# Optimization experiments

Measured on AMD Instinct MI355X. Metric: run time of the kernel, lower is better.

The kernel has to match this reference:

```python
import jax, jax.numpy as jnp
import numpy as np

B, S, D, H = 2, 2048, 1024, 16
DH = D // H  # dim_per_head = 64


def setup_inputs() -> dict:
    key = jax.random.key(0)
    ks = jax.random.split(key, 12)
    std = 1.0 / np.sqrt(D)
    inp = {
        "key": jax.random.normal(ks[0], (B, S, D), jnp.float32),
        "value": jax.random.normal(ks[1], (B, S, D), jnp.float32),
        "query": jax.random.normal(ks[2], (B, S, D), jnp.float32),
        "mask": jax.random.randint(ks[3], (B, S, S), 0, 2) == 1,
        "Wk": jax.random.normal(ks[4], (D, D), jnp.float32) * std,
        "bk": jnp.zeros((D,), jnp.float32),
        "Wv": jax.random.normal(ks[5], (D, D), jnp.float32) * std,
        "bv": jnp.zeros((D,), jnp.float32),
        "Wq": jax.random.normal(ks[6], (D, D), jnp.float32) * std,
        "bq": jnp.zeros((D,), jnp.float32),
        "Wo": jax.random.normal(ks[7], (D, D), jnp.float32) * std,
        "bo": jnp.zeros((D,), jnp.float32),
    }
    return inp


def _shape(x):
    # (B, L, D) -> (B, H, L, DH)
    return x.reshape(B, -1, H, DH).transpose(0, 2, 1, 3)


def reference(key, value, query, mask, Wk, bk, Wv, bv, Wq, bq, Wo, bo):
    k = _shape(key @ Wk.T + bk)      # (B,H,S,DH)
    v = _shape(value @ Wv.T + bv)    # (B,H,S,DH)
    q = _shape(query @ Wq.T + bq)    # (B,H,S,DH)
    q = q / jnp.sqrt(jnp.asarray(DH, q.dtype))
    scores = jnp.einsum("bhqd,bhkd->bhqk", q, k).astype(jnp.float32)
    scores = jnp.where(mask[:, None, :, :], jnp.float32(-1e18), scores)
    attn = jax.nn.softmax(scores, axis=-1).astype(q.dtype)  # (B,H,S,S)
    # dropout p=0.0 -> identity
    ctx = jnp.einsum("bhqk,bhkd->bhqd", attn, v)
    ctx = ctx.transpose(0, 2, 1, 3).reshape(B, -1, D)
    output = ctx @ Wo.T + bo
    top_attn = attn[:, 0, :, :]
    return output, top_attn
```

## Files before the change

### kernel.cpp

```cpp
#include <hip/hip_runtime.h>

constexpr int BB = 2, SS = 2048, DD = 1024, HH = 16, DHH = 64;

typedef __attribute__((ext_vector_type(4))) float f32x4;
typedef __attribute__((ext_vector_type(8))) __bf16 bf16x8;
typedef __attribute__((ext_vector_type(8))) unsigned short us8;

__device__ __forceinline__ unsigned short f32_to_bf16(float f) {
    unsigned int u = __float_as_uint(f);
    u += 0x7fffu + ((u >> 16) & 1u);
    return (unsigned short)(u >> 16);
}

__device__ __forceinline__ ushort2 pk_bf16(float a, float b) {
#if __has_builtin(__builtin_amdgcn_cvt_pk_bf16_f32)
    typedef __attribute__((ext_vector_type(2))) __bf16 bf16x2;
    bf16x2 r = __builtin_amdgcn_cvt_pk_bf16_f32(a, b);
    return *(ushort2*)&r;
#else
    ushort2 r; r.x = f32_to_bf16(a); r.y = f32_to_bf16(b); return r;
#endif
}
__device__ __forceinline__ ushort4 pk_bf16x4(float a, float b, float c, float d) {
    const ushort2 lo = pk_bf16(a, b), hi = pk_bf16(c, d);
    ushort4 r; r.x = lo.x; r.y = lo.y; r.z = hi.x; r.w = hi.y;
    return r;
}
__device__ __forceinline__ us8 cvt_us8(float4 a, float4 b) {
    const ushort4 lo = pk_bf16x4(a.x, a.y, a.z, a.w);
    const ushort4 hi = pk_bf16x4(b.x, b.y, b.z, b.w);
    us8 o;
    o[0] = lo.x; o[1] = lo.y; o[2] = lo.z; o[3] = lo.w;
    o[4] = hi.x; o[5] = hi.y; o[6] = hi.z; o[7] = hi.w;
    return o;
}

__device__ __forceinline__ f32x4 mfma_bf16(bf16x8 a, bf16x8 b, f32x4 c) {
    return __builtin_amdgcn_mfma_f32_16x16x32_bf16(a, b, c, 0, 0, 0);
}

__device__ __forceinline__ void stage16(const void* g, void* l) {
    typedef const __attribute__((address_space(1))) unsigned int gas_t;
    typedef __attribute__((address_space(3))) unsigned int las_t;
    __builtin_amdgcn_global_load_lds((gas_t*)(unsigned long long)g,
                                     (las_t*)(unsigned int)(unsigned long long)l,
                                     16, 0, 0);
}

__device__ __forceinline__ void cvt_block(const float* __restrict__ src,
                                          unsigned short* __restrict__ dst, int blk) {
    const size_t i = ((size_t)blk * 256 + threadIdx.x) * 8;
    const float4 a = *(const float4*)(src + i);
    const float4 b = *(const float4*)(src + i + 4);
    *(us8*)(dst + i) = cvt_us8(a, b);
}

__global__ __launch_bounds__(256) void cvt_bf16(const float* __restrict__ src,
                                                unsigned short* __restrict__ dst) {
    cvt_block(src, dst, blockIdx.x);
}

__global__ __launch_bounds__(256) void prep(const float* __restrict__ q,
                                            const float* __restrict__ k,
                                            const float* __restrict__ Wq,
                                            const float* __restrict__ Wk,
                                            const float* __restrict__ Wv,
                                            unsigned short* __restrict__ Xq,
                                            unsigned short* __restrict__ Xk,
                                            unsigned short* __restrict__ Wqb,
                                            unsigned short* __restrict__ Wkb,
                                            unsigned short* __restrict__ Wvb,
                                            const int* __restrict__ mask,
                                            unsigned long long* __restrict__ pm) {
    const int id = blockIdx.x;
    if (id < 4096) {
        const int sel = id >> 11, blk = id & 2047;
        cvt_block(sel == 0 ? q : k, sel == 0 ? Xq : Xk, blk);
    } else if (id < 5632) {
        const int wid = id - 4096;
        const int sel = wid >> 9, blk = wid & 511;
        cvt_block(sel == 0 ? Wq : (sel == 1 ? Wk : Wv),
                  sel == 0 ? Wqb : (sel == 1 ? Wkb : Wvb), blk);
    } else {
        const int mid = id - 5632;
        const int t = threadIdx.x, lane = t & 63;
#pragma unroll
        for (int it = 0; it < 4; ++it) {
            const size_t chunk = (size_t)mid * 16 + it * 4 + (t >> 6);
            const int val = mask[chunk * 64 + lane];
            const unsigned long long b = __ballot(val != 0);
            if (lane == 0) pm[chunk] = b;
        }
    }
}

__global__ __launch_bounds__(512) void gemm_qkv(
    const unsigned short* __restrict__ Xq, const unsigned short* __restrict__ Xk,
    const float* __restrict__ Vf,
    const unsigned short* __restrict__ Wqb, const unsigned short* __restrict__ Wkb,
    const unsigned short* __restrict__ Wvb,
    const float* __restrict__ bq, const float* __restrict__ bk,
    const float* __restrict__ bv,
    unsigned short* __restrict__ qws, unsigned short* __restrict__ kws,
    unsigned short* __restrict__ vws,
    unsigned short* __restrict__ q0, unsigned short* __restrict__ k0,
    float qscale) {
    constexpr int K = DD;
    __shared__ __align__(16) unsigned short AB[2][2][128][64];

    const int id = blockIdx.x;
    const int nid = (id & 7) * 96 + (id >> 3);
    const int which = nid >> 8;
    const int r8 = nid & 255;
    const int m0 = (r8 >> 3) * 128;
    const int n0 = (r8 & 7) * 128;

    const int t = threadIdx.x;
    const int lane = t & 63, w = t >> 6;
    const int l15 = lane & 15, quad = lane >> 4;
    const int wm = (w >> 2) * 64, wn = (w & 3) * 32;
    const bool vp = (which == 2);

    const unsigned short* Ab = which == 0 ? Xq : Xk;
    const unsigned short* Wb = which == 0 ? Wqb : (which == 1 ? Wkb : Wvb);
    const float* bias = which == 0 ? bq : (which == 1 ? bk : bv);
    const float scale = which == 0 ? qscale : 1.0f;

    const int srow = lane >> 3;
    const int scol8 = ((lane & 7) ^ srow) * 8;
    const unsigned short* Agp = Ab + (size_t)(m0 + w * 8 + srow) * K + scol8;
    const unsigned short* Bgp = Wb + (size_t)(n0 + w * 8 + srow) * K + scol8;

    const int vrow = t >> 3, vc = t & 7;
    const float* Vg = Vf + (size_t)(m0 + vrow) * K + vc * 8;

    f32x4 acc[4][2] = {};
    float4 va0, va1, va2, va3;

    if (!vp) {
#pragma unroll
        for (int j = 0; j < 2; ++j) {
            stage16(Agp + (size_t)(j * 64) * K, &AB[0][0][w * 8 + j * 64][0]);
            stage16(Bgp + (size_t)(j * 64) * K, &AB[1][0][w * 8 + j * 64][0]);
        }
    } else {
        va0 = *(const float4*)(Vg);
        va1 = *(const float4*)(Vg + 4);
        va2 = *(const float4*)(Vg + (size_t)64 * K);
        va3 = *(const float4*)(Vg + (size_t)64 * K + 4);
#pragma unroll
        for (int j = 0; j < 2; ++j)
            stage16(Bgp + (size_t)(j * 64) * K, &AB[1][0][w * 8 + j * 64][0]);
        {
            const int wr0 = vrow, wr1 = 64 + vrow;
            *(us8*)((unsigned char*)&AB[0][0][0][0] + wr0 * 128 + ((vc ^ (wr0 & 7)) * 16))
                = cvt_us8(va0, va1);
            *(us8*)((unsigned char*)&AB[0][0][0][0] + wr1 * 128 + ((vc ^ (wr1 & 7)) * 16))
                = cvt_us8(va2, va3);
        }
        __asm__ volatile("s_waitcnt lgkmcnt(0)" ::: "memory");
    }

    for (int kk = 0; kk < K / 64; ++kk) {
        const int cur = kk & 1;
        if (kk < K / 64 - 1) {
            const size_t ko = (size_t)(kk + 1) * 64;
            if (!vp) {
#pragma unroll
                for (int j = 0; j < 2; ++j) {
                    stage16(Agp + (size_t)(j * 64) * K + ko, &AB[0][cur ^ 1][w * 8 + j * 64][0]);
                    stage16(Bgp + (size_t)(j * 64) * K + ko, &AB[1][cur ^ 1][w * 8 + j * 64][0]);
                }
                __asm__ volatile("s_waitcnt vmcnt(4)" ::: "memory");
            } else {
                va0 = *(const float4*)(Vg + ko);
                va1 = *(const float4*)(Vg + ko + 4);
                va2 = *(const float4*)(Vg + (size_t)64 * K + ko);
                va3 = *(const float4*)(Vg + (size_t)64 * K + ko + 4);
#pragma unroll
                for (int j = 0; j < 2; ++j)
                    stage16(Bgp + (size_t)(j * 64) * K + ko, &AB[1][cur ^ 1][w * 8 + j * 64][0]);
                __asm__ volatile("s_waitcnt vmcnt(6)" ::: "memory");
            }
        } else {
            __asm__ volatile("s_waitcnt vmcnt(0)" ::: "memory");
        }
        __builtin_amdgcn_s_barrier();
        __builtin_amdgcn_sched_barrier(0);

#pragma unroll
        for (int s = 0; s < 2; ++s) {
            const int ch = ((s * 4 + quad) ^ (l15 & 7)) * 8;
            bf16x8 af[4], bfr[2];
#pragma unroll
            for (int mi = 0; mi < 4; ++mi)
                af[mi] = *(const bf16x8*)&AB[0][cur][wm + mi * 16 + l15][ch];
#pragma unroll
            for (int ni = 0; ni < 2; ++ni)
                bfr[ni] = *(const bf16x8*)&AB[1][cur][wn + ni * 16 + l15][ch];
            __builtin_amdgcn_s_setprio(1);
#pragma unroll
            for (int mi = 0; mi < 4; ++mi)
#pragma unroll
                for (int ni = 0; ni < 2; ++ni)
                    acc[mi][ni] = mfma_bf16(af[mi], bfr[ni], acc[mi][ni]);
            __builtin_amdgcn_s_setprio(0);
        }

        if (vp && kk < K / 64 - 1) {
            const int wr0 = vrow, wr1 = 64 + vrow;
            *(us8*)((unsigned char*)&AB[0][cur ^ 1][0][0] + wr0 * 128 + ((vc ^ (wr0 & 7)) * 16))
                = cvt_us8(va0, va1);
            *(us8*)((unsigned char*)&AB[0][cur ^ 1][0][0] + wr1 * 128 + ((vc ^ (wr1 & 7)) * 16))
                = cvt_us8(va2, va3);
            __asm__ volatile("s_waitcnt lgkmcnt(0)" ::: "memory");
        }

        __builtin_amdgcn_sched_barrier(0);
        __builtin_amdgcn_s_barrier();
        __builtin_amdgcn_sched_barrier(0);
    }

    if (which < 2) {
        unsigned short* o = which == 0 ? qws : kws;
        unsigned short* h0 = which == 0 ? q0 : k0;
#pragma unroll
        for (int ni = 0; ni < 2; ++ni) {
            const int c = n0 + wn + ni * 16 + l15;
            const float bs = bias[c];
            const int hi2 = c >> 6, di = c & (DHH - 1);
#pragma unroll
            for (int mi = 0; mi < 4; ++mi) {
#pragma unroll
                for (int r = 0; r < 4; ++r) {
                    const int mrow = m0 + wm + mi * 16 + quad * 4 + r;
                    const int bi2 = mrow >> 11, si = mrow & (SS - 1);
                    const unsigned short v16 = f32_to_bf16((acc[mi][ni][r] + bs) * scale);
                    o[((size_t)(bi2 * HH + hi2) * SS + si) * DHH + di] = v16;
                    if (hi2 == 0)
                        h0[((size_t)bi2 * SS + si) * DHH + di] = v16;
                }
            }
        }
    } else {
        unsigned short* scr = (unsigned short*)&AB[0][0][0][0] + w * (32 * 72);
#pragma unroll
        for (int ni = 0; ni < 2; ++ni) {
            const int c = n0 + wn + ni * 16 + l15;
            const float bs = bias[c];
#pragma unroll
            for (int mi = 0; mi < 4; ++mi)
                *(ushort4*)&scr[(ni * 16 + l15) * 72 + mi * 16 + quad * 4] =
                    pk_bf16x4(acc[mi][ni][0] + bs, acc[mi][ni][1] + bs,
                              acc[mi][ni][2] + bs, acc[mi][ni][3] + bs);
        }
        __asm__ volatile("s_waitcnt lgkmcnt(0)" ::: "memory");
        const int mb = m0 + wm;
        const int bi2 = mb >> 11, si0 = mb & (SS - 1);
        const int rowc = lane & 7;
#pragma unroll
        for (int k2 = 0; k2 < 4; ++k2) {
            const int col = k2 * 8 + (lane >> 3);
            const us8 vv = *(const us8*)&scr[col * 72 + rowc * 8];
            const int c = n0 + wn + col;
            *(us8*)&vws[((size_t)(bi2 * HH + (c >> 6)) * DHH + (c & 63)) * SS
                        + si0 + rowc * 8] = vv;
        }
    }
}

__global__ __launch_bounds__(512) void gemm_o(const unsigned short* __restrict__ A,
                                              const unsigned short* __restrict__ Wb,
                                              const float* __restrict__ bias,
                                              float* __restrict__ outp) {
    constexpr int K = DD;
    __shared__ __align__(16) unsigned short AB[2][2][128][64];

    const int id = blockIdx.x;
    const int nid = (id & 7) * 32 + (id >> 3);
    const int m0 = (nid >> 3) * 128;
    const int n0 = (nid & 7) * 128;

    const int t = threadIdx.x;
    const int lane = t & 63, w = t >> 6;
    const int l15 = lane & 15, quad = lane >> 4;
    const int wm = (w >> 2) * 64, wn = (w & 3) * 32;

    const int srow = lane >> 3;
    const int scol8 = ((lane & 7) ^ srow) * 8;
    const unsigned short* Agp = A + (size_t)(m0 + w * 8 + srow) * K + scol8;
    const unsigned short* Bgp = Wb + (size_t)(n0 + w * 8 + srow) * K + scol8;

    f32x4 acc[4][2] = {};

#pragma unroll
    for (int j = 0; j < 2; ++j) {
        stage16(Agp + (size_t)(j * 64) * K, &AB[0][0][w * 8 + j * 64][0]);
        stage16(Bgp + (size_t)(j * 64) * K, &AB[1][0][w * 8 + j * 64][0]);
    }

    for (int kk = 0; kk < K / 64; ++kk) {
        const int cur = kk & 1;
        if (kk < K / 64 - 1) {
            const size_t ko = (size_t)(kk + 1) * 64;
#pragma unroll
            for (int j = 0; j < 2; ++j) {
                stage16(Agp + (size_t)(j * 64) * K + ko, &AB[0][cur ^ 1][w * 8 + j * 64][0]);
                stage16(Bgp + (size_t)(j * 64) * K + ko, &AB[1][cur ^ 1][w * 8 + j * 64][0]);
            }
            __asm__ volatile("s_waitcnt vmcnt(4)" ::: "memory");
        } else {
            __asm__ volatile("s_waitcnt vmcnt(0)" ::: "memory");
        }
        __builtin_amdgcn_s_barrier();
        __builtin_amdgcn_sched_barrier(0);

#pragma unroll
        for (int s = 0; s < 2; ++s) {
            const int ch = ((s * 4 + quad) ^ (l15 & 7)) * 8;
            bf16x8 af[4], bfr[2];
#pragma unroll
            for (int mi = 0; mi < 4; ++mi)
                af[mi] = *(const bf16x8*)&AB[0][cur][wm + mi * 16 + l15][ch];
#pragma unroll
            for (int ni = 0; ni < 2; ++ni)
                bfr[ni] = *(const bf16x8*)&AB[1][cur][wn + ni * 16 + l15][ch];
            __builtin_amdgcn_s_setprio(1);
#pragma unroll
            for (int mi = 0; mi < 4; ++mi)
#pragma unroll
                for (int ni = 0; ni < 2; ++ni)
                    acc[mi][ni] = mfma_bf16(af[mi], bfr[ni], acc[mi][ni]);
            __builtin_amdgcn_s_setprio(0);
        }
        __builtin_amdgcn_sched_barrier(0);
        __builtin_amdgcn_s_barrier();
        __builtin_amdgcn_sched_barrier(0);
    }

#pragma unroll
    for (int ni = 0; ni < 2; ++ni) {
        const int c = n0 + wn + ni * 16 + l15;
        const float bs = bias[c];
#pragma unroll
        for (int mi = 0; mi < 4; ++mi)
#pragma unroll
            for (int r = 0; r < 4; ++r) {
                const int mrow = m0 + wm + mi * 16 + quad * 4 + r;
                outp[(size_t)mrow * DD + c] = acc[mi][ni][r] + bs;
            }
    }
}

__global__ __launch_bounds__(512, 4) void flash_attn(const unsigned short* __restrict__ qws,
                                                     const unsigned short* __restrict__ kws,
                                                     const unsigned short* __restrict__ vws,
                                                     const unsigned long long* __restrict__ pm,
                                                     unsigned short* __restrict__ ctx,
                                                     float2* __restrict__ stats) {
    __shared__ __align__(16) unsigned short Ksh[2][64][64];
    __shared__ __align__(16) unsigned short Vsh[2][64][64];
    __shared__ __align__(16) unsigned short Psh[8][16][72];

    constexpr int NQT = SS / 128;
    const int id = blockIdx.x;
    const int nid = (id & 7) * 64 + (id >> 3);
    const int qt = nid % NQT;
    const int bh = nid / NQT;
    const int bi = bh / HH, hi = bh % HH;

    const int t = threadIdx.x;
    const int lane = t & 63, w = t >> 6;
    const int l15 = lane & 15, quad = lane >> 4;
    const int sh4 = quad * 4;
    const int xk = quad ^ (l15 & 7);

    const unsigned short* qp = qws + (size_t)bh * SS * DHH;
    const unsigned short* kp = kws + (size_t)bh * SS * DHH;
    const unsigned short* vp = vws + (size_t)bh * DHH * SS;

    const int q_loc = qt * 128 + w * 16 + l15;
    const bf16x8 bq0 = *(const bf16x8*)(qp + (size_t)q_loc * DHH + quad * 8);
    const bf16x8 bq1 = *(const bf16x8*)(qp + (size_t)q_loc * DHH + 32 + quad * 8);
    const unsigned long long* pmrow = pm + ((size_t)bi * SS + q_loc) * (SS / 64);

    const int srow = lane >> 3;
    const int scol = (lane & 7) ^ srow;
    const unsigned short* kg = kp + (size_t)(w * 8 + srow) * DHH + scol * 8;
    const unsigned short* vg = vp + (size_t)(w * 8 + srow) * SS + scol * 8;

    f32x4 accO[4] = {};
    float m_run = -1e30f, l_run = 0.f;
    const float NEG_INF = -__builtin_inff();

    unsigned long long mcur = pmrow[0];
    stage16(kg, &Ksh[0][w * 8][0]);
    stage16(vg, &Vsh[0][w * 8][0]);

    constexpr int NT = SS / 64;
    for (int kt = 0; kt < NT; ++kt) {
        const int cur = kt & 1;
        unsigned long long mnxt = 0;
        if (kt < NT - 1) {
            mnxt = pmrow[kt + 1];
            stage16(kg + (size_t)(kt + 1) * 64 * DHH, &Ksh[cur ^ 1][w * 8][0]);
            stage16(vg + (size_t)(kt + 1) * 64,       &Vsh[cur ^ 1][w * 8][0]);
            __asm__ volatile("s_waitcnt vmcnt(3)" ::: "memory");
        } else {
            __asm__ volatile("s_waitcnt vmcnt(0)" ::: "memory");
        }
        __builtin_amdgcn_s_barrier();
        __builtin_amdgcn_sched_barrier(0);

        const unsigned short* Kb = &Ksh[cur][0][0];
        const unsigned short* Vb = &Vsh[cur][0][0];

        bf16x8 ak0[4], ak1[4];
#pragma unroll
        for (int i = 0; i < 4; ++i) {
            ak0[i] = *(const bf16x8*)&Kb[(i * 16 + l15) * 64 + xk * 8];
            ak1[i] = *(const bf16x8*)&Kb[(i * 16 + l15) * 64 + (xk ^ 4) * 8];
        }

        const unsigned int mlo = ((unsigned int)mcur) >> sh4;
        const unsigned int mhi = ((unsigned int)(mcur >> 32)) >> sh4;

        float sc[4][4];
        __builtin_amdgcn_s_setprio(1);
#pragma unroll
        for (int i = 0; i < 4; ++i) {
            f32x4 s4 = {};
            s4 = mfma_bf16(ak0[i], bq0, s4);
            s4 = mfma_bf16(ak1[i], bq1, s4);
            const unsigned int mw = (i & 2) ? mhi : mlo;
#pragma unroll
            for (int r = 0; r < 4; ++r)
                sc[i][r] = ((mw >> ((i & 1) * 16 + r)) & 1u) ? NEG_INF : s4[r];
        }
        __builtin_amdgcn_s_setprio(0);

        bf16x8 av0[4], av1[4];
#pragma unroll
        for (int i = 0; i < 4; ++i) {
            av0[i] = *(const bf16x8*)&Vb[(i * 16 + l15) * 64 + xk * 8];
            av1[i] = *(const bf16x8*)&Vb[(i * 16 + l15) * 64 + (xk ^ 4) * 8];
        }

        float tm = sc[0][0];
#pragma unroll
        for (int i = 0; i < 4; ++i)
#pragma unroll
            for (int r = 0; r < 4; ++r) tm = fmaxf(tm, sc[i][r]);
        tm = fmaxf(tm, __shfl_xor(tm, 16));
        tm = fmaxf(tm, __shfl_xor(tm, 32));

        const bool nodefer = !__all(tm <= m_run + 8.0f);
        const float mn = nodefer ? fmaxf(m_run, tm) : m_run;

        float rs = 0.f;
#pragma unroll
        for (int i = 0; i < 4; ++i)
#pragma unroll
            for (int r = 0; r < 4; ++r) {
                const float p = __builtin_amdgcn_exp2f(sc[i][r] - mn);
                sc[i][r] = p;
                rs += p;
            }
        rs += __shfl_xor(rs, 16);
        rs += __shfl_xor(rs, 32);

        if (nodefer) {
            const float alpha = __builtin_amdgcn_exp2f(m_run - mn);
            l_run = l_run * alpha + rs;
            m_run = mn;
#pragma unroll
            for (int i = 0; i < 4; ++i) accO[i] *= alpha;
        } else {
            l_run += rs;
        }

#pragma unroll
        for (int i = 0; i < 4; ++i)
            *(ushort4*)&Psh[w][l15][i * 16 + sh4] =
                pk_bf16x4(sc[i][0], sc[i][1], sc[i][2], sc[i][3]);
        __asm__ volatile("s_waitcnt lgkmcnt(0)" ::: "memory");

        const bf16x8 p0 = *(const bf16x8*)&Psh[w][l15][quad * 8];
        const bf16x8 p1 = *(const bf16x8*)&Psh[w][l15][32 + quad * 8];
        __builtin_amdgcn_s_setprio(1);
#pragma unroll
        for (int i = 0; i < 4; ++i) {
            accO[i] = mfma_bf16(av0[i], p0, accO[i]);
            accO[i] = mfma_bf16(av1[i], p1, accO[i]);
        }
        __builtin_amdgcn_s_setprio(0);

        __builtin_amdgcn_sched_barrier(0);
        __builtin_amdgcn_s_barrier();
        __builtin_amdgcn_sched_barrier(0);
        mcur = mnxt;
    }

    const float inv = 1.0f / l_run;
    unsigned short* cb = ctx + ((size_t)(bi * SS) + q_loc) * DD + hi * DHH;
#pragma unroll
    for (int i = 0; i < 4; ++i)
        *(ushort4*)&cb[i * 16 + sh4] = pk_bf16x4(accO[i][0] * inv, accO[i][1] * inv,
                                                 accO[i][2] * inv, accO[i][3] * inv);

    if (hi == 0 && quad == 0) {
        float2 st; st.x = m_run; st.y = l_run;
        stats[(size_t)bi * SS + q_loc] = st;
    }
}

__global__ __launch_bounds__(256) void prob_h0(const unsigned short* __restrict__ q0,
                                               const unsigned short* __restrict__ k0,
                                               const unsigned long long* __restrict__ pm,
                                               const float2* __restrict__ stats,
                                               float* __restrict__ outp) {
    __shared__ __align__(16) unsigned short Ksh[64][72];

    const int id = blockIdx.x;
    const int nid = (id & 7) * 64 + (id >> 3);
    const int kc = nid & 7;
    const int qt = (nid >> 3) & 31;
    const int bi = nid >> 8;

    const int t = threadIdx.x;
    const int lane = t & 63, w = t >> 6;
    const int l15 = lane & 15, quad = lane >> 4;
    const int sh4 = quad * 4;

    const int q = qt * 64 + w * 16 + l15;
    const unsigned short* qp = q0 + ((size_t)bi * SS + q) * DHH;
    const bf16x8 bq0 = *(const bf16x8*)(qp + quad * 8);
    const bf16x8 bq1 = *(const bf16x8*)(qp + 32 + quad * 8);

    const unsigned short* kp = k0 + (size_t)bi * SS * DHH;
    const unsigned long long* pmq = pm + ((size_t)bi * SS + q) * (SS / 64);
    float* orow = outp + ((size_t)bi * SS + q) * SS;

    const float2 st = stats[(size_t)bi * SS + q];
    const float M = st.x;
    const float invL = 1.0f / st.y;

    for (int kt = 0; kt < 4; ++kt) {
        const int key0 = kc * 256 + kt * 64;
        __syncthreads();
#pragma unroll
        for (int hf = 0; hf < 2; ++hf) {
            const int v = t + hf * 256;
            const int row = v >> 3, off = (v & 7) * 8;
            *(us8*)&Ksh[row][off] = *(const us8*)(kp + (size_t)(key0 + row) * DHH + off);
        }
        __syncthreads();

        const unsigned long long m64 = pmq[kc * 4 + kt];
        const unsigned int mlo = ((unsigned int)m64) >> sh4;
        const unsigned int mhi = ((unsigned int)(m64 >> 32)) >> sh4;

#pragma unroll
        for (int i = 0; i < 4; ++i) {
            const bf16x8 ak0 = *(const bf16x8*)&Ksh[i * 16 + l15][quad * 8];
            const bf16x8 ak1 = *(const bf16x8*)&Ksh[i * 16 + l15][32 + quad * 8];
            f32x4 s4 = {};
            s4 = mfma_bf16(ak0, bq0, s4);
            s4 = mfma_bf16(ak1, bq1, s4);
            const unsigned int mw = (i & 2) ? mhi : mlo;
            float4 ov;
#pragma unroll
            for (int r = 0; r < 4; ++r) {
                const float p = __builtin_amdgcn_exp2f(s4[r] - M) * invL;
                ((float*)&ov)[r] = ((mw >> ((i & 1) * 16 + r)) & 1u) ? 0.0f : p;
            }
            *(float4*)&orow[key0 + i * 16 + sh4] = ov;
        }
    }
}

extern "C" void kernel_launch(void* const* d_in, const int* in_sizes, int n_in,
                              void* d_out, int out_size, void* d_ws, size_t ws_size,
                              hipStream_t stream) {
    const float* key_   = (const float*)d_in[0];
    const float* value_ = (const float*)d_in[1];
    const float* query_ = (const float*)d_in[2];
    const int*   mask_  = (const int*)d_in[3];
    const float* Wk = (const float*)d_in[4];
    const float* bk = (const float*)d_in[5];
    const float* Wv = (const float*)d_in[6];
    const float* bv = (const float*)d_in[7];
    const float* Wq = (const float*)d_in[8];
    const float* bq = (const float*)d_in[9];
    const float* Wo = (const float*)d_in[10];
    const float* bo = (const float*)d_in[11];

    constexpr size_t XS  = (size_t)BB * SS * DD;
    constexpr size_t WSZ = (size_t)DD * DD;

    float* out_f = (float*)d_out;
    unsigned short* scratch = (unsigned short*)(out_f + XS);
    unsigned short* qws = scratch;
    unsigned short* kws = qws + XS;
    unsigned short* vws = kws + XS;
    unsigned short* ctx = vws + XS;

    unsigned short* q0 = (unsigned short*)d_ws;
    unsigned short* k0 = q0 + (size_t)BB * SS * DHH;
    unsigned long long* pm = (unsigned long long*)(k0 + (size_t)BB * SS * DHH);
    float2* stats = (float2*)(pm + (size_t)BB * SS * (SS / 64));

    unsigned short* Xq  = (unsigned short*)out_f;
    unsigned short* Xk  = Xq + XS;
    unsigned short* Wqb = ctx;
    unsigned short* Wkb = Wqb + WSZ;
    unsigned short* Wvb = Wkb + WSZ;
    unsigned short* Wob = qws;

    const float qscale = 0.125f * 1.4426950408889634f;

    prep<<<13824, 256, 0, stream>>>(query_, key_, Wq, Wk, Wv,
                                    Xq, Xk, Wqb, Wkb, Wvb, mask_, pm);

    gemm_qkv<<<768, 512, 0, stream>>>(Xq, Xk, value_, Wqb, Wkb, Wvb,
                                      bq, bk, bv, qws, kws, vws, q0, k0, qscale);

    flash_attn<<<BB * HH * (SS / 128), 512, 0, stream>>>(qws, kws, vws, pm, ctx, stats);

    cvt_bf16<<<WSZ / 2048, 256, 0, stream>>>(Wo, Wob);

    gemm_o<<<256, 512, 0, stream>>>(ctx, Wob, bo, out_f);

    prob_h0<<<512, 256, 0, stream>>>(q0, k0, pm, stats, out_f + XS);
}
```

Before: 308.9 us.

## Restructure QKV GEMM to 4-wave single-buffered tiles and split O-proj into 128x64 tiles

gemm_qkv now runs 256 threads per block with four waves, each computing a 64x64 output sub-tile (4x4 MFMA accumulators) from a single-buffered LDS tile. The intent is more blocks resident per CU (launch bounds 256,3) in place of software double buffering. gemm_o moves to 128x64 output tiles with 256 threads and 512 blocks, which fills more CUs. The cost is that global loads are no longer overlapped with MFMA inside a block; the design relies on occupancy across blocks to hide that latency.

```diff
diff --git a/kernel.cpp b/kernel.cpp
--- a/kernel.cpp
+++ b/kernel.cpp
@@ -94,7 +94,7 @@
     }
 }
 
-__global__ __launch_bounds__(512) void gemm_qkv(
+__global__ __launch_bounds__(256, 3) void gemm_qkv(
     const unsigned short* __restrict__ Xq, const unsigned short* __restrict__ Xk,
     const float* __restrict__ Vf,
     const unsigned short* __restrict__ Wqb, const unsigned short* __restrict__ Wkb,
@@ -106,7 +106,9 @@
     unsigned short* __restrict__ q0, unsigned short* __restrict__ k0,
     float qscale) {
     constexpr int K = DD;
-    __shared__ __align__(16) unsigned short AB[2][2][128][64];
+    __shared__ __align__(16) unsigned char LDSU[36864];
+    unsigned short* Ash = (unsigned short*)LDSU;
+    unsigned short* Bsh = Ash + 128 * 64;
 
     const int id = blockIdx.x;
     const int nid = (id & 7) * 96 + (id >> 3);
@@ -116,74 +118,51 @@
     const int n0 = (r8 & 7) * 128;
 
     const int t = threadIdx.x;
-    const int lane = t & 63, w = t >> 6;
+    const int lane = t & 63;
     const int l15 = lane & 15, quad = lane >> 4;
-    const int wm = (w >> 2) * 64, wn = (w & 3) * 32;
+    const int w = t >> 6, wr = w >> 1, wc = w & 1;
     const bool vp = (which == 2);
 
-    const unsigned short* Ab = which == 0 ? Xq : Xk;
+    const unsigned short* Ap = which == 0 ? Xq : Xk;
     const unsigned short* Wb = which == 0 ? Wqb : (which == 1 ? Wkb : Wvb);
     const float* bias = which == 0 ? bq : (which == 1 ? bk : bv);
     const float scale = which == 0 ? qscale : 1.0f;
 
-    const int srow = lane >> 3;
-    const int scol8 = ((lane & 7) ^ srow) * 8;
-    const unsigned short* Agp = Ab + (size_t)(m0 + w * 8 + srow) * K + scol8;
-    const unsigned short* Bgp = Wb + (size_t)(n0 + w * 8 + srow) * K + scol8;
-
-    const int vrow = t >> 3, vc = t & 7;
-    const float* Vg = Vf + (size_t)(m0 + vrow) * K + vc * 8;
-
-    f32x4 acc[4][2] = {};
-    float4 va0, va1, va2, va3;
-
-    if (!vp) {
-#pragma unroll
-        for (int j = 0; j < 2; ++j) {
-            stage16(Agp + (size_t)(j * 64) * K, &AB[0][0][w * 8 + j * 64][0]);
-            stage16(Bgp + (size_t)(j * 64) * K, &AB[1][0][w * 8 + j * 64][0]);
-        }
-    } else {
-        va0 = *(const float4*)(Vg);
-        va1 = *(const float4*)(Vg + 4);
-        va2 = *(const float4*)(Vg + (size_t)64 * K);
-        va3 = *(const float4*)(Vg + (size_t)64 * K + 4);
-#pragma unroll
-        for (int j = 0; j < 2; ++j)
-            stage16(Bgp + (size_t)(j * 64) * K, &AB[1][0][w * 8 + j * 64][0]);
-        {
-            const int wr0 = vrow, wr1 = 64 + vrow;
-            *(us8*)((unsigned char*)&AB[0][0][0][0] + wr0 * 128 + ((vc ^ (wr0 & 7)) * 16))
-                = cvt_us8(va0, va1);
-            *(us8*)((unsigned char*)&AB[0][0][0][0] + wr1 * 128 + ((vc ^ (wr1 & 7)) * 16))
-                = cvt_us8(va2, va3);
-        }
-        __asm__ volatile("s_waitcnt lgkmcnt(0)" ::: "memory");
-    }
+    const int srow = t >> 3;
+    const int scol8 = ((t & 7) ^ (srow & 7)) * 8;
+    const unsigned short* Agp = Ap + (size_t)(m0 + srow) * K + scol8;
+    const unsigned short* Bgp = Wb + (size_t)(n0 + srow) * K + scol8;
+    const float* Vgp = Vf + (size_t)(m0 + srow) * K + scol8;
+    char* ldst = (char*)LDSU + t * 16;
+
+    f32x4 acc[4][4] = {};
 
     for (int kk = 0; kk < K / 64; ++kk) {
-        const int cur = kk & 1;
-        if (kk < K / 64 - 1) {
-            const size_t ko = (size_t)(kk + 1) * 64;
-            if (!vp) {
-#pragma unroll
-                for (int j = 0; j < 2; ++j) {
-                    stage16(Agp + (size_t)(j * 64) * K + ko, &AB[0][cur ^ 1][w * 8 + j * 64][0]);
-                    stage16(Bgp + (size_t)(j * 64) * K + ko, &AB[1][cur ^ 1][w * 8 + j * 64][0]);
-                }
-                __asm__ volatile("s_waitcnt vmcnt(4)" ::: "memory");
-            } else {
-                va0 = *(const float4*)(Vg + ko);
-                va1 = *(const float4*)(Vg + ko + 4);
-                va2 = *(const float4*)(Vg + (size_t)64 * K + ko);
-                va3 = *(const float4*)(Vg + (size_t)64 * K + ko + 4);
-#pragma unroll
-                for (int j = 0; j < 2; ++j)
-                    stage16(Bgp + (size_t)(j * 64) * K + ko, &AB[1][cur ^ 1][w * 8 + j * 64][0]);
-                __asm__ volatile("s_waitcnt vmcnt(6)" ::: "memory");
+        const size_t ko = (size_t)kk * 64;
+        if (!vp) {
+#pragma unroll
+            for (int j = 0; j < 4; ++j)
+                stage16(Agp + (size_t)(j * 32) * K + ko, ldst + j * 4096);
+#pragma unroll
+            for (int j = 0; j < 4; ++j)
+                stage16(Bgp + (size_t)(j * 32) * K + ko, ldst + 16384 + j * 4096);
+            __asm__ volatile("s_waitcnt vmcnt(0)" ::: "memory");
+        } else {
+            float4 va[8];
+#pragma unroll
+            for (int j = 0; j < 4; ++j) {
+                const float* vsrc = Vgp + (size_t)(j * 32) * K + ko;
+                va[2 * j]     = *(const float4*)vsrc;
+                va[2 * j + 1] = *(const float4*)(vsrc + 4);
             }
-        } else {
+#pragma unroll
+            for (int j = 0; j < 4; ++j)
+                stage16(Bgp + (size_t)(j * 32) * K + ko, ldst + 16384 + j * 4096);
             __asm__ volatile("s_waitcnt vmcnt(0)" ::: "memory");
+#pragma unroll
+            for (int j = 0; j < 4; ++j)
+                *(us8*)(ldst + j * 4096) = cvt_us8(va[2 * j], va[2 * j + 1]);
+            __asm__ volatile("s_waitcnt lgkmcnt(0)" ::: "memory");
         }
         __builtin_amdgcn_s_barrier();
         __builtin_amdgcn_sched_barrier(0);
@@ -191,31 +170,21 @@
 #pragma unroll
         for (int s = 0; s < 2; ++s) {
             const int ch = ((s * 4 + quad) ^ (l15 & 7)) * 8;
-            bf16x8 af[4], bfr[2];
+            bf16x8 af[4], bfr[4];
 #pragma unroll
             for (int mi = 0; mi < 4; ++mi)
-                af[mi] = *(const bf16x8*)&AB[0][cur][wm + mi * 16 + l15][ch];
-#pragma unroll
-            for (int ni = 0; ni < 2; ++ni)
-                bfr[ni] = *(const bf16x8*)&AB[1][cur][wn + ni * 16 + l15][ch];
+                af[mi] = *(const bf16x8*)&Ash[(wr * 64 + mi * 16 + l15) * 64 + ch];
+#pragma unroll
+            for (int ni = 0; ni < 4; ++ni)
+                bfr[ni] = *(const bf16x8*)&Bsh[(wc * 64 + ni * 16 + l15) * 64 + ch];
             __builtin_amdgcn_s_setprio(1);
 #pragma unroll
             for (int mi = 0; mi < 4; ++mi)
 #pragma unroll
-                for (int ni = 0; ni < 2; ++ni)
+                for (int ni = 0; ni < 4; ++ni)
                     acc[mi][ni] = mfma_bf16(af[mi], bfr[ni], acc[mi][ni]);
             __builtin_amdgcn_s_setprio(0);
         }
-
-        if (vp && kk < K / 64 - 1) {
-            const int wr0 = vrow, wr1 = 64 + vrow;
-            *(us8*)((unsigned char*)&AB[0][cur ^ 1][0][0] + wr0 * 128 + ((vc ^ (wr0 & 7)) * 16))
-                = cvt_us8(va0, va1);
-            *(us8*)((unsigned char*)&AB[0][cur ^ 1][0][0] + wr1 * 128 + ((vc ^ (wr1 & 7)) * 16))
-                = cvt_us8(va2, va3);
-            __asm__ volatile("s_waitcnt lgkmcnt(0)" ::: "memory");
-        }
-
         __builtin_amdgcn_sched_barrier(0);
         __builtin_amdgcn_s_barrier();
         __builtin_amdgcn_sched_barrier(0);
@@ -225,15 +194,15 @@
         unsigned short* o = which == 0 ? qws : kws;
         unsigned short* h0 = which == 0 ? q0 : k0;
 #pragma unroll
-        for (int ni = 0; ni < 2; ++ni) {
-            const int c = n0 + wn + ni * 16 + l15;
+        for (int ni = 0; ni < 4; ++ni) {
+            const int c = n0 + wc * 64 + ni * 16 + l15;
             const float bs = bias[c];
             const int hi2 = c >> 6, di = c & (DHH - 1);
 #pragma unroll
             for (int mi = 0; mi < 4; ++mi) {
 #pragma unroll
                 for (int r = 0; r < 4; ++r) {
-                    const int mrow = m0 + wm + mi * 16 + quad * 4 + r;
+                    const int mrow = m0 + wr * 64 + mi * 16 + quad * 4 + r;
                     const int bi2 = mrow >> 11, si = mrow & (SS - 1);
                     const unsigned short v16 = f32_to_bf16((acc[mi][ni][r] + bs) * scale);
                     o[((size_t)(bi2 * HH + hi2) * SS + si) * DHH + di] = v16;
@@ -243,77 +212,78 @@
             }
         }
     } else {
-        unsigned short* scr = (unsigned short*)&AB[0][0][0][0] + w * (32 * 72);
-#pragma unroll
-        for (int ni = 0; ni < 2; ++ni) {
-            const int c = n0 + wn + ni * 16 + l15;
-            const float bs = bias[c];
+        unsigned short* scr = (unsigned short*)LDSU + w * (64 * 68);
+#pragma unroll
+        for (int ni = 0; ni < 4; ++ni) {
+            const float bs = bias[n0 + wc * 64 + ni * 16 + l15];
 #pragma unroll
             for (int mi = 0; mi < 4; ++mi)
-                *(ushort4*)&scr[(ni * 16 + l15) * 72 + mi * 16 + quad * 4] =
+                *(ushort4*)&scr[(ni * 16 + l15) * 68 + mi * 16 + quad * 4] =
                     pk_bf16x4(acc[mi][ni][0] + bs, acc[mi][ni][1] + bs,
                               acc[mi][ni][2] + bs, acc[mi][ni][3] + bs);
         }
         __asm__ volatile("s_waitcnt lgkmcnt(0)" ::: "memory");
-        const int mb = m0 + wm;
+        const int mb = m0 + wr * 64;
         const int bi2 = mb >> 11, si0 = mb & (SS - 1);
-        const int rowc = lane & 7;
-#pragma unroll
-        for (int k2 = 0; k2 < 4; ++k2) {
-            const int col = k2 * 8 + (lane >> 3);
-            const us8 vv = *(const us8*)&scr[col * 72 + rowc * 8];
-            const int c = n0 + wn + col;
+        const int rowc = lane & 7, colg = lane >> 3;
+#pragma unroll
+        for (int k2 = 0; k2 < 8; ++k2) {
+            const int col = k2 * 8 + colg;
+            const us8 vv = *(const us8*)&scr[col * 68 + rowc * 8];
+            const int c = n0 + wc * 64 + col;
             *(us8*)&vws[((size_t)(bi2 * HH + (c >> 6)) * DHH + (c & 63)) * SS
                         + si0 + rowc * 8] = vv;
         }
     }
 }
 
-__global__ __launch_bounds__(512) void gemm_o(const unsigned short* __restrict__ A,
-                                              const unsigned short* __restrict__ Wb,
-                                              const float* __restrict__ bias,
-                                              float* __restrict__ outp) {
+__device__ __forceinline__ void gemm_body(const unsigned short* __restrict__ A,
+                                          const unsigned short* __restrict__ Wb,
+                                          const float* __restrict__ bias,
+                                          float* __restrict__ outp, int nid) {
     constexpr int K = DD;
-    __shared__ __align__(16) unsigned short AB[2][2][128][64];
-
-    const int id = blockIdx.x;
-    const int nid = (id & 7) * 32 + (id >> 3);
-    const int m0 = (nid >> 3) * 128;
-    const int n0 = (nid & 7) * 128;
+    __shared__ __align__(16) unsigned short Ash[2][128][64];
+    __shared__ __align__(16) unsigned short Bsh[2][64][64];
+
+    const int n0 = (nid & 15) * 64;
+    const int m0 = (nid >> 4) * 128;
 
     const int t = threadIdx.x;
     const int lane = t & 63, w = t >> 6;
     const int l15 = lane & 15, quad = lane >> 4;
-    const int wm = (w >> 2) * 64, wn = (w & 3) * 32;
+    const int wm = (w >> 1) * 64, wn = (w & 1) * 32;
 
     const int srow = lane >> 3;
     const int scol8 = ((lane & 7) ^ srow) * 8;
-    const unsigned short* Agp = A + (size_t)(m0 + w * 8 + srow) * K + scol8;
-    const unsigned short* Bgp = Wb + (size_t)(n0 + w * 8 + srow) * K + scol8;
+    const unsigned short* Ag = A + (size_t)(m0 + w * 32 + srow) * K + scol8;
+    const unsigned short* Bg = Wb + (size_t)(n0 + w * 16 + srow) * K + scol8;
 
     f32x4 acc[4][2] = {};
 
 #pragma unroll
-    for (int j = 0; j < 2; ++j) {
-        stage16(Agp + (size_t)(j * 64) * K, &AB[0][0][w * 8 + j * 64][0]);
-        stage16(Bgp + (size_t)(j * 64) * K, &AB[1][0][w * 8 + j * 64][0]);
-    }
+    for (int j = 0; j < 4; ++j) stage16(Ag + (size_t)j * 8 * K, &Ash[0][w * 32 + j * 8][0]);
+#pragma unroll
+    for (int j = 0; j < 2; ++j) stage16(Bg + (size_t)j * 8 * K, &Bsh[0][w * 16 + j * 8][0]);
 
     for (int kk = 0; kk < K / 64; ++kk) {
         const int cur = kk & 1;
         if (kk < K / 64 - 1) {
             const size_t ko = (size_t)(kk + 1) * 64;
 #pragma unroll
-            for (int j = 0; j < 2; ++j) {
-                stage16(Agp + (size_t)(j * 64) * K + ko, &AB[0][cur ^ 1][w * 8 + j * 64][0]);
-                stage16(Bgp + (size_t)(j * 64) * K + ko, &AB[1][cur ^ 1][w * 8 + j * 64][0]);
-            }
-            __asm__ volatile("s_waitcnt vmcnt(4)" ::: "memory");
+            for (int j = 0; j < 4; ++j)
+                stage16(Ag + (size_t)j * 8 * K + ko, &Ash[cur ^ 1][w * 32 + j * 8][0]);
+#pragma unroll
+            for (int j = 0; j < 2; ++j)
+                stage16(Bg + (size_t)j * 8 * K + ko, &Bsh[cur ^ 1][w * 16 + j * 8][0]);
+            __asm__ volatile("s_waitcnt vmcnt(6)" ::: "memory");
         } else {
             __asm__ volatile("s_waitcnt vmcnt(0)" ::: "memory");
         }
         __builtin_amdgcn_s_barrier();
         __builtin_amdgcn_sched_barrier(0);
+
+        const unsigned short* Ab = &Ash[cur][0][0];
+        const unsigned short* Bb = &Bsh[cur][0][0];
 
 #pragma unroll
         for (int s = 0; s < 2; ++s) {
@@ -321,10 +291,10 @@
             bf16x8 af[4], bfr[2];
 #pragma unroll
             for (int mi = 0; mi < 4; ++mi)
-                af[mi] = *(const bf16x8*)&AB[0][cur][wm + mi * 16 + l15][ch];
+                af[mi] = *(const bf16x8*)&Ab[(wm + mi * 16 + l15) * 64 + ch];
 #pragma unroll
             for (int ni = 0; ni < 2; ++ni)
-                bfr[ni] = *(const bf16x8*)&AB[1][cur][wn + ni * 16 + l15][ch];
+                bfr[ni] = *(const bf16x8*)&Bb[(wn + ni * 16 + l15) * 64 + ch];
             __builtin_amdgcn_s_setprio(1);
 #pragma unroll
             for (int mi = 0; mi < 4; ++mi)
@@ -350,6 +320,15 @@
                 outp[(size_t)mrow * DD + c] = acc[mi][ni][r] + bs;
             }
     }
+}
+
+__global__ __launch_bounds__(256) void gemm_o(const unsigned short* __restrict__ A,
+                                              const unsigned short* __restrict__ Wb,
+                                              const float* __restrict__ bias,
+                                              float* __restrict__ outp) {
+    const int id = blockIdx.x;
+    const int nid = (id & 7) * 64 + (id >> 3);
+    gemm_body(A, Wb, bias, outp, nid);
 }
 
 __global__ __launch_bounds__(512, 4) void flash_attn(const unsigned short* __restrict__ qws,
@@ -622,14 +601,14 @@
     prep<<<13824, 256, 0, stream>>>(query_, key_, Wq, Wk, Wv,
                                     Xq, Xk, Wqb, Wkb, Wvb, mask_, pm);
 
-    gemm_qkv<<<768, 512, 0, stream>>>(Xq, Xk, value_, Wqb, Wkb, Wvb,
+    gemm_qkv<<<768, 256, 0, stream>>>(Xq, Xk, value_, Wqb, Wkb, Wvb,
                                       bq, bk, bv, qws, kws, vws, q0, k0, qscale);
 
     flash_attn<<<BB * HH * (SS / 128), 512, 0, stream>>>(qws, kws, vws, pm, ctx, stats);
 
     cvt_bf16<<<WSZ / 2048, 256, 0, stream>>>(Wo, Wob);
 
-    gemm_o<<<256, 512, 0, stream>>>(ctx, Wob, bo, out_f);
+    gemm_o<<<512, 256, 0, stream>>>(ctx, Wob, bo, out_f);
 
     prob_h0<<<512, 256, 0, stream>>>(q0, k0, pm, stats, out_f + XS);
 }
```

Result: slower. 321.8 us (+4.2%).
